# Optimization experiments

Measured on AMD Instinct MI355X. Metric: run time of the kernel, lower is better.

## Reference

```python
import jax, jax.numpy as jnp
import numpy as np
import math

C = 128
A_SCALES = [2.0, 4.0, 8.0]
A_RATIOS = [0.5, 1.0, 2.0]
STRIDES = [4, 8, 16, 32, 64]
NA = len(A_SCALES) * len(A_RATIOS)
IMG = 1024
N = 2
NMS_THRESH = 0.7
NUM_PRE = 6000
NUM_POST = 300
SCALE_CLIP = math.log(1000.0 / 16.0)


def base_anchors(stride):
    c = stride / 2.0
    a = []
    for s in A_SCALES:
        for r in A_RATIOS:
            h = stride * s * math.sqrt(r)
            w = stride * s * math.sqrt(1.0 / r)
            a.append((c - h / 2.0, c - w / 2.0, c + h / 2.0, c + w / 2.0))
    return np.array(a, dtype=np.float32)  # [NA,4] yxyx


def shifted_anchors(stride, H, W):
    base = jnp.asarray(base_anchors(stride))
    gy = jnp.arange(H, dtype=jnp.float32) * stride
    gx = jnp.arange(W, dtype=jnp.float32) * stride
    grid = jnp.stack(jnp.meshgrid(gy, gx, indexing='ij'), axis=-1)  # [H,W,2]
    shift = jnp.concatenate([grid, grid], axis=-1)  # [H,W,4]
    return (base[None, None] + shift[:, :, None]).reshape(-1, 4)  # [H*W*NA,4]


def conv(x, w, b, pad):
    y = jax.lax.conv_general_dilated(x, w, (1, 1), pad, dimension_numbers=('NCHW', 'OIHW', 'NCHW'))
    return y + b[None, :, None, None]


def head(x, w1, b1, wobj, bobj, wbbx, bbbx):
    h = jax.nn.relu(conv(x, w1, b1, 'SAME'))
    obj = conv(h, wobj, bobj, 'VALID')  # [N,NA,H,W]
    bbx = conv(h, wbbx, bbbx, 'VALID')  # [N,4*NA,H,W]
    n = x.shape[0]
    obj = obj.transpose(0, 2, 3, 1).reshape(n, -1)       # (h,w,anchor) order
    bbx = bbx.transpose(0, 2, 3, 1).reshape(n, -1, 4)
    return obj, bbx


def shift_boxes(anchors, deltas):
    yx = (anchors[..., :2] + anchors[..., 2:]) * 0.5
    hw = anchors[..., 2:] - anchors[..., :2]
    yx_o = yx + deltas[..., :2] * hw
    hw_o = hw * jnp.exp(jnp.minimum(deltas[..., 2:], SCALE_CLIP))
    return jnp.concatenate([yx_o - 0.5 * hw_o, yx_o + 0.5 * hw_o], axis=-1)


def nms_single(boxes, scores):
    # greedy hard NMS; boxes [P,4] yxyx, scores [P]; fixed NUM_POST outputs
    areas = (boxes[:, 2] - boxes[:, 0]) * (boxes[:, 3] - boxes[:, 1])

    def step(active, _):
        masked = jnp.where(active, scores, -jnp.inf)
        i = jnp.argmax(masked)
        ok = active[i]
        tl = jnp.maximum(boxes[i, :2], boxes[:, :2])
        br = jnp.minimum(boxes[i, 2:], boxes[:, 2:])
        inter = jnp.clip(br[:, 0] - tl[:, 0], 0.0) * jnp.clip(br[:, 1] - tl[:, 1], 0.0)
        iou = inter / (areas[i] + areas - inter + 1e-9)
        active = active & (iou <= NMS_THRESH)
        return active, (jnp.where(ok, i, 0), ok)

    _, (idx, valid) = jax.lax.scan(step, jnp.ones(boxes.shape[0], bool), None, length=NUM_POST)
    return idx, valid


def forward(x0, x1, x2, x3, x4, w1, b1, wobj, bobj, wbbx, bbbx, valid_size):
    feats = [x0, x1, x2, x3, x4]
    objs, bbxs, ancs = [], [], []
    for f, s in zip(feats, STRIDES):
        o, b = head(f, w1, b1, wobj, bobj, wbbx, bbbx)
        objs.append(o)
        bbxs.append(b)
        ancs.append(shifted_anchors(s, f.shape[2], f.shape[3]))
    obj = jnp.concatenate(objs, axis=1)        # [N,M]
    bbx = jnp.concatenate(bbxs, axis=1)        # [N,M,4]
    anchors = jnp.concatenate(ancs, axis=0)    # [M,4]
    boxes = shift_boxes(anchors[None], bbx)    # [N,M,4]
    h = valid_size[:, 0].astype(boxes.dtype)[:, None]
    w = valid_size[:, 1].astype(boxes.dtype)[:, None]
    boxes = jnp.stack([jnp.clip(boxes[..., 0], 0.0, h),
                       jnp.clip(boxes[..., 1], 0.0, w),
                       jnp.clip(boxes[..., 2], 0.0, h),
                       jnp.clip(boxes[..., 3], 0.0, w)], axis=-1)
    k = min(boxes.shape[1], NUM_PRE)
    top_scores, top_idx = jax.lax.top_k(obj, k)                     # per-image topk
    top_boxes = jnp.take_along_axis(boxes, top_idx[..., None], axis=1)
    idx, valid = jax.vmap(nms_single)(jax.lax.stop_gradient(top_boxes),
                                      jax.lax.stop_gradient(top_scores))
    props = jnp.take_along_axis(top_boxes, idx[..., None], axis=1)  # [N,NUM_POST,4]
    props = props * valid[..., None].astype(props.dtype)            # zero-pad invalid
    return props, valid


def setup_inputs() -> dict:
    key = jax.random.key(0)
    ks = jax.random.split(key, 8)
    sizes = [IMG // s for s in STRIDES]
    inp = {}
    for i, hw in enumerate(sizes):
        inp['x%d' % i] = jax.random.normal(ks[i], (N, C, hw, hw), jnp.float32)
    inp['w1'] = jax.random.normal(ks[5], (C, C, 3, 3), jnp.float32) * 0.05
    inp['b1'] = jnp.zeros((C,), jnp.float32)
    inp['wobj'] = jax.random.normal(ks[6], (NA, C, 1, 1), jnp.float32) * 0.05
    inp['bobj'] = jnp.zeros((NA,), jnp.float32)
    inp['wbbx'] = jax.random.normal(ks[7], (4 * NA, C, 1, 1), jnp.float32) * 0.05
    inp['bbbx'] = jnp.zeros((4 * NA,), jnp.float32)
    inp['valid_size'] = jnp.array([[IMG, IMG]] * N, jnp.int32)
    return inp


def reference(x0, x1, x2, x3, x4, w1, b1, wobj, bobj, wbbx, bbbx, valid_size):
    return forward(x0, x1, x2, x3, x4, w1, b1, wobj, bobj, wbbx, bbbx, valid_size)
```

## Files before the change

### kernel.cpp

```cpp
#include <hip/hip_runtime.h>
#include <stdint.h>
#include <math.h>

#define M_TOT 785664
#define NPRE  6000
#define NPOST 300
#define CAP   8192
#define NWORDS 94
#define ROWW   96
#define NPAD   6016

__device__ __forceinline__ uint32_t okey(float f) {
    uint32_t u = __float_as_uint(f);
    return (u & 0x80000000u) ? ~u : (u | 0x80000000u);
}

__global__ void k_zero(uint32_t* p, int n) {
    int i = blockIdx.x * blockDim.x + threadIdx.x;
    if (i < n) p[i] = 0u;
}

__global__ void k_wt(const float* __restrict__ w1, float* __restrict__ wt) {
    int i = blockIdx.x * 256 + threadIdx.x;
    if (i >= 128 * 128 * 9) return;
    int co = i / 1152; int r = i % 1152; int ci = r / 9; int tap = r % 9;
    wt[ci * 1152 + tap * 128 + co] = w1[i];
}

__global__ __launch_bounds__(512) void k_conv(
    const float* __restrict__ x0, const float* __restrict__ x1,
    const float* __restrict__ x2, const float* __restrict__ x3,
    const float* __restrict__ x4,
    const float* __restrict__ wt, const float* __restrict__ b1,
    const float* __restrict__ wobj, const float* __restrict__ bobj,
    const float* __restrict__ wbbx, const float* __restrict__ bbbx,
    float* __restrict__ sc, float* __restrict__ dl)
{
    __shared__ __attribute__((aligned(16))) float sx[8][18][20];
    __shared__ __attribute__((aligned(16))) float sw[8 * 9 * 128];

    int b = blockIdx.x, L = 0;
    if (b >= 512) { b -= 512; L = 1;
        if (b >= 128) { b -= 128; L = 2;
            if (b >= 32) { b -= 32; L = 3;
                if (b >= 8) { b -= 8; L = 4; } } } }
    const float* xs = (L == 0) ? x0 : (L == 1) ? x1 : (L == 2) ? x2 : (L == 3) ? x3 : x4;
    const int scoff_[5] = {0, 589824, 737280, 774144, 783360};
    int Wl = 256 >> L; int Hl = Wl; int HW = Wl * Wl;
    int tpiSh = 8 - 2 * L;
    int n  = b >> tpiSh;
    int r  = b & ((1 << tpiSh) - 1);
    int txSh = 4 - L;
    int ty0 = r >> txSh, tx0 = r & ((1 << txSh) - 1);
    int y0 = ty0 << 4, x0c = tx0 << 4;
    const float* xin = xs + (size_t)n * 128 * HW;

    int t = threadIdx.x;
    int tx = t & 15;
    int ty = t >> 4;
    int py = ty >> 1, px = (ty & 1) << 3;

    float acc0[4][8], acc1[4][8];
#pragma unroll
    for (int c = 0; c < 4; ++c)
#pragma unroll
        for (int e = 0; e < 8; ++e) { acc0[c][e] = 0.f; acc1[c][e] = 0.f; }

    for (int cc0 = 0; cc0 < 128; cc0 += 8) {
        __syncthreads();
        for (int i = t; i < 2880; i += 512) {
            int ci = i / 360; int rm = i % 360; int rr = rm / 20; int cc = rm % 20;
            float v = 0.f;
            int gy = y0 - 1 + rr, gx = x0c - 1 + cc;
            if (cc < 18 && gy >= 0 && gy < Hl && gx >= 0 && gx < Wl)
                v = xin[(size_t)(cc0 + ci) * HW + (size_t)gy * Wl + gx];
            sx[ci][rr][cc] = v;
        }
        {
            const float4* wsrc = (const float4*)(wt + (size_t)cc0 * 1152);
            float4* wdst = (float4*)sw;
            for (int i = t; i < 2304; i += 512) wdst[i] = wsrc[i];
        }
        __syncthreads();

#pragma unroll 1
        for (int ci = 0; ci < 8; ++ci) {
#pragma unroll
            for (int dy = 0; dy < 3; ++dy) {
                const float* xr = &sx[ci][py + dy][px];
                float4 xa = *(const float4*)(xr);
                float4 xb = *(const float4*)(xr + 4);
                float4 xc = *(const float4*)(xr + 8);
                float win[12] = {xa.x, xa.y, xa.z, xa.w, xb.x, xb.y, xb.z, xb.w,
                                 xc.x, xc.y, xc.z, xc.w};
#pragma unroll
                for (int dx = 0; dx < 3; ++dx) {
                    const float* wr = &sw[(ci * 9 + dy * 3 + dx) * 128 + tx * 4];
                    float4 wa = *(const float4*)(wr);
                    float4 wb = *(const float4*)(wr + 64);
                    float wva[4] = {wa.x, wa.y, wa.z, wa.w};
                    float wvb[4] = {wb.x, wb.y, wb.z, wb.w};
#pragma unroll
                    for (int e = 0; e < 8; ++e) {
                        float xv = win[e + dx];
#pragma unroll
                        for (int c = 0; c < 4; ++c) {
                            acc0[c][e] = fmaf(wva[c], xv, acc0[c][e]);
                            acc1[c][e] = fmaf(wvb[c], xv, acc1[c][e]);
                        }
                    }
                }
            }
        }
    }

#pragma unroll
    for (int c = 0; c < 4; ++c) {
        float ba = b1[tx * 4 + c];
        float bb = b1[64 + tx * 4 + c];
#pragma unroll
        for (int e = 0; e < 8; ++e) {
            float v0 = acc0[c][e] + ba;
            float v1 = acc1[c][e] + bb;
            acc0[c][e] = v0 > 0.f ? v0 : 0.f;
            acc1[c][e] = v1 > 0.f ? v1 : 0.f;
        }
    }

    int gy = y0 + py;
    size_t ppos = (size_t)gy * Wl + x0c + px;
    size_t scbase = (size_t)n * M_TOT + scoff_[L];
    size_t dlbase = (size_t)n * 4 * (size_t)M_TOT + 4 * (size_t)scoff_[L];
    for (int a = 0; a < 45; ++a) {
        const float* wp = (a < 9) ? (wobj + (size_t)a * 128) : (wbbx + (size_t)(a - 9) * 128);
        float4 wa = *(const float4*)(wp + tx * 4);
        float4 wb = *(const float4*)(wp + 64 + tx * 4);
        float wva[4] = {wa.x, wa.y, wa.z, wa.w};
        float wvb[4] = {wb.x, wb.y, wb.z, wb.w};
        float p[8];
#pragma unroll
        for (int e = 0; e < 8; ++e) p[e] = 0.f;
#pragma unroll
        for (int c = 0; c < 4; ++c)
#pragma unroll
            for (int e = 0; e < 8; ++e) {
                p[e] = fmaf(wva[c], acc0[c][e], p[e]);
                p[e] = fmaf(wvb[c], acc1[c][e], p[e]);
            }
#pragma unroll
        for (int mm = 1; mm < 16; mm <<= 1)
#pragma unroll
            for (int e = 0; e < 8; ++e)
                p[e] += __shfl_xor(p[e], mm, 64);
        if (tx == 0) {
            float bias = (a < 9) ? bobj[a] : bbbx[a - 9];
            float4 o0 = make_float4(p[0] + bias, p[1] + bias, p[2] + bias, p[3] + bias);
            float4 o1 = make_float4(p[4] + bias, p[5] + bias, p[6] + bias, p[7] + bias);
            float* dst = (a < 9) ? (sc + scbase + (size_t)a * HW + ppos)
                                 : (dl + dlbase + (size_t)(a - 9) * HW + ppos);
            *(float4*)dst = o0;
            *(float4*)(dst + 4) = o1;
        }
    }
}

__global__ __launch_bounds__(256) void k_hist(const float* __restrict__ sc,
                                              uint32_t* __restrict__ hist) {
    __shared__ uint32_t lh[8192];
    int n = blockIdx.y;
    for (int i = threadIdx.x; i < 8192; i += 256) lh[i] = 0u;
    __syncthreads();
    const float* s = sc + (size_t)n * M_TOT;
    int stride = gridDim.x * 256;
    for (int i = blockIdx.x * 256 + threadIdx.x; i < M_TOT; i += stride)
        atomicAdd(&lh[okey(s[i]) >> 19], 1u);
    __syncthreads();
    for (int i = threadIdx.x; i < 8192; i += 256) {
        uint32_t v = lh[i];
        if (v) atomicAdd(&hist[n * 8192 + i], v);
    }
}

__global__ void k_subhist(const float* __restrict__ sc, const uint32_t* __restrict__ ctrl,
                          uint32_t* __restrict__ subh) {
    int i = blockIdx.x * blockDim.x + threadIdx.x;
    int stride = gridDim.x * blockDim.x;
    for (; i < 2 * M_TOT; i += stride) {
        int n = i >= M_TOT;
        uint32_t k = okey(sc[i]);
        if ((k >> 19) == ctrl[n * 8 + 0])
            atomicAdd(&subh[n * 8192 + ((k >> 6) & 0x1FFFu)], 1u);
    }
}

__global__ void k_scan(const uint32_t* __restrict__ hist, uint32_t* __restrict__ ctrl, int phase) {
    int n = blockIdx.x;
    const uint32_t* h = hist + n * 8192;
    uint32_t* c = ctrl + n * 8;
    __shared__ uint32_t tp[256];
    int t = threadIdx.x;
    uint32_t s = 0;
    for (int r = 0; r < 32; ++r) s += h[8191 - (t * 32 + r)];
    tp[t] = s;
    __syncthreads();
    if (t == 0) {
        uint32_t run = (phase == 0) ? 0u : c[1];
        for (int i = 0; i < 256; ++i) { uint32_t v = tp[i]; tp[i] = run; run += v; }
    }
    __syncthreads();
    uint32_t cum = tp[t];
    for (int r = 0; r < 32; ++r) {
        int j = 8191 - (t * 32 + r);
        uint32_t cc = h[j];
        if (cum < 6000u && cum + cc >= 6000u) {
            if (phase == 0) { c[0] = (uint32_t)j; c[1] = cum; }
            else            { c[2] = (c[0] << 19) | ((uint32_t)j << 6); }
        }
        cum += cc;
    }
}

__global__ void k_compact(const float* __restrict__ sc, uint32_t* __restrict__ ctrl,
                          uint64_t* __restrict__ cand) {
    int i = blockIdx.x * blockDim.x + threadIdx.x;
    int stride = gridDim.x * blockDim.x;
    const int scoff_[5] = {0, 589824, 737280, 774144, 783360};
    int lane = threadIdx.x & 63;
    for (; i < 2 * M_TOT; i += stride) {
        int n = i >= M_TOT;
        int q = n ? (i - M_TOT) : i;
        uint32_t k = okey(sc[i]);
        bool hit = (k >= ctrl[n * 8 + 2]);
        unsigned long long m = __ballot(hit);
        if (m) {
            int leader = __builtin_ctzll(m);
            uint32_t base = 0;
            if (lane == leader) base = atomicAdd(&ctrl[n * 8 + 3], (uint32_t)__popcll(m));
            base = (uint32_t)__shfl((int)base, leader, 64);
            if (hit) {
                uint32_t slot = base + (uint32_t)__popcll(m & ((1ull << lane) - 1ull));
                if (slot < CAP) {
                    int Lq = (q < 589824) ? 0 : (q < 737280) ? 1 : (q < 774144) ? 2
                            : (q < 783360) ? 3 : 4;
                    int r = q - scoff_[Lq];
                    int sh = 16 - 2 * Lq;
                    int a = r >> sh;
                    int pos = r & ((1 << sh) - 1);
                    uint32_t mm = (uint32_t)(scoff_[Lq] + pos * 9 + a);
                    cand[(size_t)n * CAP + slot] = ((uint64_t)k << 32) | (uint32_t)(~mm);
                }
            }
        }
    }
}

__global__ __launch_bounds__(256) void k_rank(const uint64_t* __restrict__ cand,
                                              const uint32_t* __restrict__ ctrl,
                                              uint64_t* __restrict__ sorted) {
    __shared__ uint64_t chunk[2048];
    int n = blockIdx.y;
    uint32_t cnt = ctrl[n * 8 + 3];
    if (cnt > CAP) cnt = CAP;
    const uint64_t* cb = cand + (size_t)n * CAP;
    uint64_t* sb = sorted + (size_t)n * CAP;
    int i = blockIdx.x * 256 + threadIdx.x;
    uint64_t key = (i < (int)cnt) ? cb[i] : 0ull;
    uint32_t rank = 0;
    for (uint32_t base = 0; base < cnt; base += 2048) {
        __syncthreads();
        for (int j = threadIdx.x; j < 2048; j += 256) {
            uint32_t idx = base + (uint32_t)j;
            chunk[j] = (idx < cnt) ? cb[idx] : 0ull;
        }
        __syncthreads();
        uint32_t lim = cnt - base; if (lim > 2048u) lim = 2048u;
        for (uint32_t j = 0; j < lim; ++j) rank += (chunk[j] > key) ? 1u : 0u;
    }
    if (i < (int)cnt && rank < CAP) sb[rank] = key;
}

__global__ void k_decode(const uint64_t* __restrict__ cand, const float* __restrict__ dl,
                         const int* __restrict__ vsz, float* __restrict__ boxes) {
    int i = blockIdx.x * 256 + threadIdx.x;
    if (i >= 2 * NPRE) return;
    int n = i / NPRE, rk = i % NPRE;
    const int scoff_[5] = {0, 589824, 737280, 774144, 783360};
    uint64_t pk = cand[(size_t)n * CAP + rk];
    uint32_t m = ~(uint32_t)(pk & 0xFFFFFFFFull);
    int Lq = (m < 589824u) ? 0 : (m < 737280u) ? 1 : (m < 774144u) ? 2 : (m < 783360u) ? 3 : 4;
    int r = (int)m - scoff_[Lq];
    int pos = r / 9;
    int a = r - pos * 9;
    int Wl = 256 >> Lq;
    int y = pos >> (8 - Lq);
    int xx = pos & (Wl - 1);
    float stridef = (float)(4 << Lq);
    double sD = (double)(2 << (a / 3));
    double rD = ((a % 3) == 0) ? 0.5 : ((a % 3) == 1) ? 1.0 : 2.0;
    double hD = ((double)stridef * sD) * sqrt(rD);
    double wD = ((double)stridef * sD) * sqrt(1.0 / rD);
    double cD = (double)stridef / 2.0;
    float y1b = (float)(cD - hD / 2.0);
    float x1b = (float)(cD - wD / 2.0);
    float y2b = (float)(cD + hD / 2.0);
    float x2b = (float)(cD + wD / 2.0);
    float gy = (float)y * stridef;
    float gx = (float)xx * stridef;
    float ay1 = __fadd_rn(y1b, gy), ax1 = __fadd_rn(x1b, gx);
    float ay2 = __fadd_rn(y2b, gy), ax2 = __fadd_rn(x2b, gx);
    float cy = __fmul_rn(__fadd_rn(ay1, ay2), 0.5f);
    float cx = __fmul_rn(__fadd_rn(ax1, ax2), 0.5f);
    float ah = __fsub_rn(ay2, ay1);
    float aw = __fsub_rn(ax2, ax1);
    size_t HWl = (size_t)Wl * Wl;
    size_t db = (size_t)n * 4 * M_TOT + 4 * (size_t)scoff_[Lq] + (size_t)pos;
    float dy_ = dl[db + (size_t)(a * 4 + 0) * HWl];
    float dx_ = dl[db + (size_t)(a * 4 + 1) * HWl];
    float dh_ = dl[db + (size_t)(a * 4 + 2) * HWl];
    float dw_ = dl[db + (size_t)(a * 4 + 3) * HWl];
    float yo = __fadd_rn(cy, __fmul_rn(dy_, ah));
    float xo = __fadd_rn(cx, __fmul_rn(dx_, aw));
    const float SCLIPf = 4.135166556742356f;
    float ho = __fmul_rn(ah, (float)exp((double)fminf(dh_, SCLIPf)));
    float wo = __fmul_rn(aw, (float)exp((double)fminf(dw_, SCLIPf)));
    float hf = (float)vsz[n * 2 + 0], wf = (float)vsz[n * 2 + 1];
    float y1 = fminf(fmaxf(__fsub_rn(yo, __fmul_rn(0.5f, ho)), 0.f), hf);
    float x1 = fminf(fmaxf(__fsub_rn(xo, __fmul_rn(0.5f, wo)), 0.f), wf);
    float y2 = fminf(fmaxf(__fadd_rn(yo, __fmul_rn(0.5f, ho)), 0.f), hf);
    float x2 = fminf(fmaxf(__fadd_rn(xo, __fmul_rn(0.5f, wo)), 0.f), wf);
    *(float4*)(boxes + ((size_t)n * NPAD + rk) * 4) = make_float4(y1, x1, y2, x2);
}

__global__ __launch_bounds__(256) void k_iou(const float* __restrict__ boxes,
                                             uint64_t* __restrict__ ioum) {
    int n = blockIdx.y;
    int i = blockIdx.x * 4 + (threadIdx.x >> 6);
    int lane = threadIdx.x & 63;
    const float* bsrc = boxes + (size_t)n * NPAD * 4;
    float4 bi = *(const float4*)(bsrc + (size_t)i * 4);
    float ai = __fmul_rn(__fsub_rn(bi.z, bi.x), __fsub_rn(bi.w, bi.y));
    uint64_t* row = ioum + ((size_t)n * NPAD + i) * ROWW;
    int w0 = i >> 6;
    for (int w = lane; w < w0; w += 64) row[w] = 0ull;
    for (int w = w0; w < NWORDS; ++w) {
        int j = (w << 6) | lane;
        bool pred = false;
        if (j > i && j < NPRE) {
            float4 bj = *(const float4*)(bsrc + (size_t)j * 4);
            float aj = __fmul_rn(__fsub_rn(bj.z, bj.x), __fsub_rn(bj.w, bj.y));
            float ty = fmaxf(bi.x, bj.x), tx2 = fmaxf(bi.y, bj.y);
            float by = fminf(bi.z, bj.z), bx2 = fminf(bi.w, bj.w);
            float ih = fmaxf(__fsub_rn(by, ty), 0.f), iw = fmaxf(__fsub_rn(bx2, tx2), 0.f);
            float inter = __fmul_rn(ih, iw);
            float den = __fadd_rn(__fsub_rn(__fadd_rn(ai, aj), inter), 1e-9f);
            float iou = __fdiv_rn(inter, den);
            pred = iou > 0.7f;
        }
        unsigned long long msk = __ballot(pred);
        if (lane == 0) row[w] = (uint64_t)msk;
    }
}

__global__ __launch_bounds__(64) void k_nms(const float* __restrict__ boxes,
                                            const uint64_t* __restrict__ ioum,
                                            float* __restrict__ out) {
    int n = blockIdx.x;
    __shared__ uint64_t sup[NWORDS];
    __shared__ int keepl[NPOST];
    int lane = threadIdx.x;
    for (int w = lane; w < NWORDS; w += 64) sup[w] = 0ull;
    __syncthreads();
    int kept = 0;
    bool stop = false;
    for (int w = 0; w < NWORDS && kept < NPOST && !stop; ++w) {
        uint64_t vmask = (w == NWORDS - 1) ? ((1ull << 48) - 1ull) : ~0ull;
        uint64_t avail = (~sup[w]) & vmask;
        while (avail && kept < NPOST) {
            int bpos = __builtin_ctzll(avail);
            int i = (w << 6) | bpos;
            if (lane == 0) keepl[kept] = i;
            kept++;
            float4 bi = *(const float4*)(boxes + ((size_t)n * NPAD + i) * 4);
            float area = __fmul_rn(__fsub_rn(bi.z, bi.x), __fsub_rn(bi.w, bi.y));
            float selfiou = __fdiv_rn(area, __fadd_rn(area, 1e-9f));
            if (!(selfiou > 0.7f)) {
                if (lane == 0) { for (int k2 = kept; k2 < NPOST; ++k2) keepl[k2] = i; }
                kept = NPOST;
                stop = true;
                break;
            }
            const uint64_t* row = ioum + ((size_t)n * NPAD + i) * ROWW;
            sup[lane] |= row[lane];
            if (lane < NWORDS - 64) sup[64 + lane] |= row[64 + lane];
            __syncthreads();
            avail = (~sup[w]) & vmask & ~((2ull << bpos) - 1ull);
        }
    }
    __syncthreads();
    for (int k = lane; k < NPOST; k += 64) {
        float4 bx = make_float4(0.f, 0.f, 0.f, 0.f);
        float vf = 0.f;
        if (k < kept) {
            int i = keepl[k];
            bx = *(const float4*)(boxes + ((size_t)n * NPAD + i) * 4);
            vf = 1.f;
        }
        *(float4*)(out + (size_t)n * 1200 + (size_t)k * 4) = bx;
        out[2400 + n * 300 + k] = vf;
    }
}

__global__ __launch_bounds__(256) void k_diag(const uint32_t* __restrict__ ctrl,
                                              const uint64_t* __restrict__ sorted,
                                              const float* __restrict__ boxes,
                                              float* __restrict__ out) {
    __shared__ unsigned sfl;
    if (threadIdx.x == 0) sfl = 0u;
    __syncthreads();
    unsigned fl = 0;
    for (int n = 0; n < 2; ++n) {
        if (threadIdx.x == 0) {
            uint32_t cnt = ctrl[n * 8 + 3];
            if (cnt < 6000u || cnt > (uint32_t)CAP) fl |= 1u << n;
        }
        for (int r = threadIdx.x + 1; r < NPRE; r += 256)
            if (sorted[(size_t)n * CAP + r - 1] <= sorted[(size_t)n * CAP + r])
                fl |= 4u << n;
        for (int r = threadIdx.x; r < NPRE * 4; r += 256) {
            float v = boxes[(size_t)n * NPAD * 4 + r];
            if (!(v >= 0.0f && v <= 1024.0f)) fl |= 16u << n;
        }
    }
    if (fl) atomicOr(&sfl, fl);
    __syncthreads();
    if (threadIdx.x == 0 && sfl) out[0] = 65536.0f * (float)(1u + sfl);
}

extern "C" void kernel_launch(void* const* d_in, const int* in_sizes, int n_in,
                              void* d_out, int out_size, void* d_ws, size_t ws_size,
                              hipStream_t stream) {
    (void)out_size; (void)ws_size;
    static const int want[12] = {16777216, 4194304, 1048576, 262144, 65536,
                                 147456, 128, 1152, 9, 4608, 36, 4};
    const void* p[12];
    for (int k = 0; k < 12; ++k) p[k] = d_in[k];
    bool pos_ok = (n_in >= 12);
    for (int k = 0; k < 12 && pos_ok; ++k) if (in_sizes[k] != want[k]) pos_ok = false;
    if (!pos_ok) {
        for (int k = 0; k < 12; ++k)
            for (int j = 0; j < n_in; ++j)
                if (in_sizes[j] == want[k]) { p[k] = d_in[j]; break; }
    }
    const float* x0   = (const float*)p[0];
    const float* x1   = (const float*)p[1];
    const float* x2   = (const float*)p[2];
    const float* x3   = (const float*)p[3];
    const float* x4   = (const float*)p[4];
    const float* w1   = (const float*)p[5];
    const float* b1   = (const float*)p[6];
    const float* wobj = (const float*)p[7];
    const float* bobj = (const float*)p[8];
    const float* wbbx = (const float*)p[9];
    const float* bbbx = (const float*)p[10];
    const int*   vsz  = (const int*)p[11];
    float* out = (float*)d_out;

    size_t off = 0;
    char* base = (char*)d_ws;
    auto carve = [&](size_t bytes) -> void* {
        void* q = base + off;
        off += (bytes + 255) & ~(size_t)255;
        return q;
    };
    float*    SC     = (float*)carve((size_t)2 * M_TOT * 4);
    float*    DL     = (float*)carve((size_t)2 * M_TOT * 16);
    float*    WT     = (float*)carve((size_t)147456 * 4);
    uint32_t* HIST   = (uint32_t*)carve((size_t)16384 * 4);
    uint32_t* SUBH   = (uint32_t*)carve((size_t)16384 * 4);
    uint32_t* CTRL   = (uint32_t*)carve((size_t)64 * 4);
    uint64_t* CAND   = (uint64_t*)carve((size_t)2 * CAP * 8);
    uint64_t* SORTED = (uint64_t*)carve((size_t)2 * CAP * 8);
    float*    BOXES  = (float*)carve((size_t)2 * NPAD * 16);
    uint64_t* IOUM   = (uint64_t*)carve((size_t)2 * NPAD * ROWW * 8);

    int zn = (int)(((char*)CAND - (char*)HIST) / 4);
    k_zero<<<(zn + 255) / 256, 256, 0, stream>>>(HIST, zn);
    k_wt<<<(147456 + 255) / 256, 256, 0, stream>>>(w1, WT);
    k_conv<<<682, 512, 0, stream>>>(x0, x1, x2, x3, x4, WT, b1,
                                    wobj, bobj, wbbx, bbbx, SC, DL);
    k_hist<<<dim3(256, 2), 256, 0, stream>>>(SC, HIST);
    k_scan<<<2, 256, 0, stream>>>(HIST, CTRL, 0);
    k_subhist<<<1024, 256, 0, stream>>>(SC, CTRL, SUBH);
    k_scan<<<2, 256, 0, stream>>>(SUBH, CTRL, 1);
    k_compact<<<1024, 256, 0, stream>>>(SC, CTRL, CAND);
    k_rank<<<dim3(CAP / 256, 2), 256, 0, stream>>>(CAND, CTRL, SORTED);
    k_decode<<<(2 * NPRE + 255) / 256, 256, 0, stream>>>(SORTED, DL, vsz, BOXES);
    k_iou<<<dim3(NPRE / 4, 2), 256, 0, stream>>>(BOXES, IOUM);
    k_nms<<<2, 64, 0, stream>>>(BOXES, IOUM, out);
    k_diag<<<1, 256, 0, stream>>>(CTRL, SORTED, BOXES, out);
}
```

Baseline: 1.095 ms.

## Precompute degenerate-box mask, prefetch NMS rows, drop diag kernel, unroll conv

Three unrelated changes. The decode kernel now computes each box's self-IoU test and sets a bit in a degenerate-box bitmask, so the serial NMS loop reads a shared-memory bit instead of loading the box and doing a divide. The NMS loop also issues its suppression-row loads before the bookkeeping, and the diagnostic validation kernel is removed, saving one launch. The conv inner channel loop is unrolled by 2, which may raise register pressure. DEGM sits inside the zeroed HIST..CAND region, so it is cleared each call.

```diff
diff --git a/kernel.cpp b/kernel.cpp
--- a/kernel.cpp
+++ b/kernel.cpp
@@ -83,7 +83,7 @@
         }
         __syncthreads();
 
-#pragma unroll 1
+#pragma unroll 2
         for (int ci = 0; ci < 8; ++ci) {
 #pragma unroll
             for (int dy = 0; dy < 3; ++dy) {
@@ -280,7 +280,8 @@
 }
 
 __global__ void k_decode(const uint64_t* __restrict__ cand, const float* __restrict__ dl,
-                         const int* __restrict__ vsz, float* __restrict__ boxes) {
+                         const int* __restrict__ vsz, float* __restrict__ boxes,
+                         unsigned long long* __restrict__ degm) {
     int i = blockIdx.x * 256 + threadIdx.x;
     if (i >= 2 * NPRE) return;
     int n = i / NPRE, rk = i % NPRE;
@@ -329,6 +330,10 @@
     float y2 = fminf(fmaxf(__fadd_rn(yo, __fmul_rn(0.5f, ho)), 0.f), hf);
     float x2 = fminf(fmaxf(__fadd_rn(xo, __fmul_rn(0.5f, wo)), 0.f), wf);
     *(float4*)(boxes + ((size_t)n * NPAD + rk) * 4) = make_float4(y1, x1, y2, x2);
+    float area = __fmul_rn(__fsub_rn(y2, y1), __fsub_rn(x2, x1));
+    float selfiou = __fdiv_rn(area, __fadd_rn(area, 1e-9f));
+    if (!(selfiou > 0.7f))
+        atomicOr(&degm[(size_t)n * ROWW + (rk >> 6)], 1ull << (rk & 63));
 }
 
 __global__ __launch_bounds__(256) void k_iou(const float* __restrict__ boxes,
@@ -363,12 +368,17 @@
 
 __global__ __launch_bounds__(64) void k_nms(const float* __restrict__ boxes,
                                             const uint64_t* __restrict__ ioum,
+                                            const unsigned long long* __restrict__ degm,
                                             float* __restrict__ out) {
     int n = blockIdx.x;
     __shared__ uint64_t sup[NWORDS];
+    __shared__ uint64_t deg[NWORDS];
     __shared__ int keepl[NPOST];
     int lane = threadIdx.x;
-    for (int w = lane; w < NWORDS; w += 64) sup[w] = 0ull;
+    for (int w = lane; w < NWORDS; w += 64) {
+        sup[w] = 0ull;
+        deg[w] = degm[(size_t)n * ROWW + w];
+    }
     __syncthreads();
     int kept = 0;
     bool stop = false;
@@ -378,20 +388,19 @@
         while (avail && kept < NPOST) {
             int bpos = __builtin_ctzll(avail);
             int i = (w << 6) | bpos;
+            const uint64_t* row = ioum + ((size_t)n * NPAD + i) * ROWW;
+            uint64_t r0 = row[lane];
+            uint64_t r1 = (lane < NWORDS - 64) ? row[64 + lane] : 0ull;
             if (lane == 0) keepl[kept] = i;
             kept++;
-            float4 bi = *(const float4*)(boxes + ((size_t)n * NPAD + i) * 4);
-            float area = __fmul_rn(__fsub_rn(bi.z, bi.x), __fsub_rn(bi.w, bi.y));
-            float selfiou = __fdiv_rn(area, __fadd_rn(area, 1e-9f));
-            if (!(selfiou > 0.7f)) {
+            if ((deg[w] >> bpos) & 1ull) {
                 if (lane == 0) { for (int k2 = kept; k2 < NPOST; ++k2) keepl[k2] = i; }
                 kept = NPOST;
                 stop = true;
                 break;
             }
-            const uint64_t* row = ioum + ((size_t)n * NPAD + i) * ROWW;
-            sup[lane] |= row[lane];
-            if (lane < NWORDS - 64) sup[64 + lane] |= row[64 + lane];
+            sup[lane] |= r0;
+            if (lane < NWORDS - 64) sup[64 + lane] |= r1;
             __syncthreads();
             avail = (~sup[w]) & vmask & ~((2ull << bpos) - 1ull);
         }
@@ -408,32 +417,6 @@
         *(float4*)(out + (size_t)n * 1200 + (size_t)k * 4) = bx;
         out[2400 + n * 300 + k] = vf;
     }
-}
-
-__global__ __launch_bounds__(256) void k_diag(const uint32_t* __restrict__ ctrl,
-                                              const uint64_t* __restrict__ sorted,
-                                              const float* __restrict__ boxes,
-                                              float* __restrict__ out) {
-    __shared__ unsigned sfl;
-    if (threadIdx.x == 0) sfl = 0u;
-    __syncthreads();
-    unsigned fl = 0;
-    for (int n = 0; n < 2; ++n) {
-        if (threadIdx.x == 0) {
-            uint32_t cnt = ctrl[n * 8 + 3];
-            if (cnt < 6000u || cnt > (uint32_t)CAP) fl |= 1u << n;
-        }
-        for (int r = threadIdx.x + 1; r < NPRE; r += 256)
-            if (sorted[(size_t)n * CAP + r - 1] <= sorted[(size_t)n * CAP + r])
-                fl |= 4u << n;
-        for (int r = threadIdx.x; r < NPRE * 4; r += 256) {
-            float v = boxes[(size_t)n * NPAD * 4 + r];
-            if (!(v >= 0.0f && v <= 1024.0f)) fl |= 16u << n;
-        }
-    }
-    if (fl) atomicOr(&sfl, fl);
-    __syncthreads();
-    if (threadIdx.x == 0 && sfl) out[0] = 65536.0f * (float)(1u + sfl);
 }
 
 extern "C" void kernel_launch(void* const* d_in, const int* in_sizes, int n_in,
@@ -478,6 +461,7 @@
     uint32_t* HIST   = (uint32_t*)carve((size_t)16384 * 4);
     uint32_t* SUBH   = (uint32_t*)carve((size_t)16384 * 4);
     uint32_t* CTRL   = (uint32_t*)carve((size_t)64 * 4);
+    unsigned long long* DEGM = (unsigned long long*)carve((size_t)2 * ROWW * 8);
     uint64_t* CAND   = (uint64_t*)carve((size_t)2 * CAP * 8);
     uint64_t* SORTED = (uint64_t*)carve((size_t)2 * CAP * 8);
     float*    BOXES  = (float*)carve((size_t)2 * NPAD * 16);
@@ -494,8 +478,7 @@
     k_scan<<<2, 256, 0, stream>>>(SUBH, CTRL, 1);
     k_compact<<<1024, 256, 0, stream>>>(SC, CTRL, CAND);
     k_rank<<<dim3(CAP / 256, 2), 256, 0, stream>>>(CAND, CTRL, SORTED);
-    k_decode<<<(2 * NPRE + 255) / 256, 256, 0, stream>>>(SORTED, DL, vsz, BOXES);
+    k_decode<<<(2 * NPRE + 255) / 256, 256, 0, stream>>>(SORTED, DL, vsz, BOXES, DEGM);
     k_iou<<<dim3(NPRE / 4, 2), 256, 0, stream>>>(BOXES, IOUM);
-    k_nms<<<2, 64, 0, stream>>>(BOXES, IOUM, out);
-    k_diag<<<1, 256, 0, stream>>>(CTRL, SORTED, BOXES, out);
-}
+    k_nms<<<2, 64, 0, stream>>>(BOXES, IOUM, DEGM, out);
+}
```

New measurement: 1.163 ms. 6.2% more time.
